# Performance work log

Measured on AMD Instinct MI355X. Metric: run time of the kernel, lower is better.

Reference implementation:

```python
import jax, jax.numpy as jnp
import numpy as np

DIM = 1024
HEADS = 16
WIN = 7
HEAD_DIM = DIM // HEADS
SCALE = HEAD_DIM ** -0.5
B = 1024
N = WIN * WIN  # 49 tokens per window


def _relative_position_index(window_size: int) -> np.ndarray:
    coords = np.stack(np.meshgrid(np.arange(window_size), np.arange(window_size), indexing='ij'))
    cf = coords.reshape(2, -1)  # [2, N]
    rel = cf[:, :, None] - cf[:, None, :]  # [2, N, N]
    rel = rel.transpose(1, 2, 0)
    rel[:, :, 0] += window_size - 1
    rel[:, :, 1] += window_size - 1
    rel[:, :, 0] *= 2 * window_size - 1
    return rel.sum(-1).astype(np.int32)  # [N, N]


def setup_inputs() -> dict:
    key = jax.random.key(0)
    ks = jax.random.split(key, 12)
    s = 0.02
    inp = {
        'landmark_features': jax.random.normal(ks[0], (B, N, DIM), jnp.float32),
        'image_features': jax.random.normal(ks[1], (B, N, DIM), jnp.float32),
        'Wq': jax.random.normal(ks[2], (DIM, DIM), jnp.float32) * s,
        'bq': jnp.zeros((DIM,), jnp.float32),
        'Wk': jax.random.normal(ks[3], (DIM, DIM), jnp.float32) * s,
        'bk': jnp.zeros((DIM,), jnp.float32),
        'Wv': jax.random.normal(ks[4], (DIM, DIM), jnp.float32) * s,
        'bv': jnp.zeros((DIM,), jnp.float32),
        'Wo': jax.random.normal(ks[5], (DIM, DIM), jnp.float32) * s,
        'bo': jnp.zeros((DIM,), jnp.float32),
        'bias_table': jax.random.normal(ks[6], ((2 * WIN - 1) ** 2, HEADS), jnp.float32) * s,
        'rel_idx': jnp.asarray(_relative_position_index(WIN)),
    }
    return inp


def reference(landmark_features, image_features, Wq, bq, Wk, bk, Wv, bv, Wo, bo, bias_table, rel_idx):
    Bsz, Nk, C = image_features.shape
    # projections (torch Linear: x @ W.T + b), split into heads -> [B, H, N, D]
    def proj(x, W, b):
        y = x @ W.T + b
        return y.reshape(Bsz, -1, HEADS, HEAD_DIM).transpose(0, 2, 1, 3)
    q = proj(landmark_features, Wq, bq)
    k = proj(image_features, Wk, bk)
    v = proj(image_features, Wv, bv)
    attn = jnp.einsum('bhqd,bhkd->bhqk', q, k) * SCALE
    # gathered relative-position bias: [H, N, N]
    bias = bias_table[rel_idx.reshape(-1)].reshape(N, N, HEADS).transpose(2, 0, 1)
    attn = attn + bias[None]
    attn = jax.nn.softmax(attn, axis=-1)
    out = jnp.einsum('bhqk,bhkd->bhqd', attn, v).transpose(0, 2, 1, 3).reshape(Bsz, -1, C)
    return out @ Wo.T + bo
```

## Files before the change

kernel.cpp:

```cpp
#include <hip/hip_runtime.h>

#define DIM 1024
#define HEADS 16
#define HEAD_DIM 64
#define NTOK 49
#define SCALEF 0.125f

typedef __attribute__((ext_vector_type(8))) short bf16x8;
typedef __attribute__((ext_vector_type(4))) float floatx4;

typedef const __attribute__((address_space(1))) void* gptr_t;
typedef __attribute__((address_space(3))) void* sptr_t;

__device__ __forceinline__ void async_load16(const void* g, void* s) {
    __builtin_amdgcn_global_load_lds((gptr_t)g, (sptr_t)s, 16, 0, 0);
}

__device__ __forceinline__ unsigned short f2bf(float f) {
    unsigned int u = __builtin_bit_cast(unsigned int, f);
    u = (u + 0x7fffu + ((u >> 16) & 1u)) >> 16;
    return (unsigned short)u;
}
__device__ __forceinline__ float bf2f(unsigned short s) {
    unsigned int u = ((unsigned int)s) << 16;
    return __builtin_bit_cast(float, u);
}

__global__ void cvt2_kernel(const float* __restrict__ a, const float* __restrict__ b,
                            unsigned short* __restrict__ oa, unsigned short* __restrict__ ob,
                            int n) {
    int i = (blockIdx.x * 256 + threadIdx.x) * 4;
    if (i >= n) return;
    float4 va = *(const float4*)&a[i];
    float4 vb = *(const float4*)&b[i];
    ushort4 ua = make_ushort4(f2bf(va.x), f2bf(va.y), f2bf(va.z), f2bf(va.w));
    ushort4 ub = make_ushort4(f2bf(vb.x), f2bf(vb.y), f2bf(vb.z), f2bf(vb.w));
    *(ushort4*)&oa[i] = ua;
    *(ushort4*)&ob[i] = ub;
}

template <bool OUT_BF16>
__global__ __launch_bounds__(256)
void gemm_bt_kernel(const unsigned short* __restrict__ A,
                    const unsigned short* __restrict__ Bw,
                    const float* __restrict__ bias,
                    void* __restrict__ Cout) {
    constexpr int K = 1024, N = 1024;
    __shared__ unsigned short As[128 * 32];
    __shared__ unsigned short Bs[128 * 32];
    const int tid = threadIdx.x;
    const int lane = tid & 63;
    const int wave = tid >> 6;
    const int wm = (wave >> 1) * 64;
    const int wn = (wave & 1) * 64;
    const int m0 = blockIdx.y * 128;
    const int n0 = blockIdx.x * 128;
    const int lr = lane & 15;
    const int lk = (lane >> 4) * 8;

    floatx4 acc[4][4] = {};

    for (int kt = 0; kt < K / 32; ++kt) {
        const int kbase = kt * 32;
#pragma unroll
        for (int j = 0; j < 2; ++j) {
            int off = tid * 16 + j * 4096;
            int r = off >> 6;
            int ce = (off & 63) >> 1;
            async_load16(A + (size_t)(m0 + r) * K + kbase + ce, (char*)As + off);
            async_load16(Bw + (size_t)(n0 + r) * K + kbase + ce, (char*)Bs + off);
        }
        __syncthreads();
        bf16x8 af[4], bfr[4];
#pragma unroll
        for (int t = 0; t < 4; ++t) {
            af[t]  = *(const bf16x8*)&As[(wm + t * 16 + lr) * 32 + lk];
            bfr[t] = *(const bf16x8*)&Bs[(wn + t * 16 + lr) * 32 + lk];
        }
#pragma unroll
        for (int mt = 0; mt < 4; ++mt)
#pragma unroll
            for (int nt = 0; nt < 4; ++nt)
                acc[mt][nt] = __builtin_amdgcn_mfma_f32_16x16x32_bf16(
                    af[mt], bfr[nt], acc[mt][nt], 0, 0, 0);
        __syncthreads();
    }

#pragma unroll
    for (int mt = 0; mt < 4; ++mt) {
#pragma unroll
        for (int nt = 0; nt < 4; ++nt) {
            int col = n0 + wn + nt * 16 + (lane & 15);
            float bv = bias[col];
#pragma unroll
            for (int r = 0; r < 4; ++r) {
                int row = m0 + wm + mt * 16 + (lane >> 4) * 4 + r;
                float v = acc[mt][nt][r] + bv;
                if (OUT_BF16)
                    ((unsigned short*)Cout)[(size_t)row * N + col] = f2bf(v);
                else
                    ((float*)Cout)[(size_t)row * N + col] = v;
            }
        }
    }
}

__global__ void bias_pre_kernel(const float* __restrict__ bias_table,
                                const int* __restrict__ rel_idx,
                                float* __restrict__ bias_dense) {
    int h = blockIdx.x;
    for (int i = threadIdx.x; i < 64 * 64; i += 256) {
        int q = i >> 6, k = i & 63;
        float v;
        if (k >= NTOK) v = -1e30f;
        else if (q >= NTOK) v = 0.f;
        else v = bias_table[rel_idx[q * NTOK + k] * HEADS + h];
        bias_dense[h * 4096 + i] = v;
    }
}

#define SWZ(row, t) ((t) ^ (((row) & 7) << 3))

__global__ __launch_bounds__(256)
void attn_mfma_kernel(const unsigned short* __restrict__ Q,
                      const unsigned short* __restrict__ K,
                      const unsigned short* __restrict__ V,
                      const float* __restrict__ bias_dense,
                      unsigned short* __restrict__ ctx) {
    __shared__ unsigned short Vt[4][64 * 64];
    __shared__ unsigned short Pm[4][64 * 64];

    const int tid = threadIdx.x;
    const int w = tid >> 6;
    const int lane = tid & 63;
    const int p = blockIdx.x * 4 + w;
    const int b = p >> 4;
    const int h = p & 15;
    const size_t base = (size_t)(b * NTOK) * DIM + h * HEAD_DIM;
    unsigned short* vt = Vt[w];
    unsigned short* pm = Pm[w];

    const int lc = lane & 15;
    const int lg = lane >> 4;

    for (int i = lane; i < 64 * 16; i += 64) {
        int tok = i >> 4, d0 = (i & 15) * 4;
        ushort4 vv = (tok < NTOK) ? *(const ushort4*)&V[base + (size_t)tok * DIM + d0]
                                  : make_ushort4(0, 0, 0, 0);
        vt[(d0 + 0) * 64 + SWZ(d0 + 0, tok)] = vv.x;
        vt[(d0 + 1) * 64 + SWZ(d0 + 1, tok)] = vv.y;
        vt[(d0 + 2) * 64 + SWZ(d0 + 2, tok)] = vv.z;
        vt[(d0 + 3) * 64 + SWZ(d0 + 3, tok)] = vv.w;
    }

    floatx4 acc[4][4] = {};
#pragma unroll
    for (int kt = 0; kt < 2; ++kt) {
        const int d = kt * 32 + lg * 8;
        bf16x8 af[4], bfr[4];
#pragma unroll
        for (int mt = 0; mt < 4; ++mt)
            af[mt] = *(const bf16x8*)&Q[base + (size_t)(mt * 16 + lc) * DIM + d];
#pragma unroll
        for (int nt = 0; nt < 4; ++nt)
            bfr[nt] = *(const bf16x8*)&K[base + (size_t)(nt * 16 + lc) * DIM + d];
#pragma unroll
        for (int mt = 0; mt < 4; ++mt)
#pragma unroll
            for (int nt = 0; nt < 4; ++nt)
                acc[mt][nt] = __builtin_amdgcn_mfma_f32_16x16x32_bf16(
                    af[mt], bfr[nt], acc[mt][nt], 0, 0, 0);
    }

    const float* bd = bias_dense + h * 4096;
#pragma unroll
    for (int mt = 0; mt < 4; ++mt) {
#pragma unroll
        for (int r = 0; r < 4; ++r) {
            const int row = mt * 16 + lg * 4 + r;
#pragma unroll
            for (int nt = 0; nt < 4; ++nt)
                acc[mt][nt][r] = acc[mt][nt][r] * SCALEF + bd[row * 64 + nt * 16 + lc];
            float mx = fmaxf(fmaxf(acc[mt][0][r], acc[mt][1][r]),
                             fmaxf(acc[mt][2][r], acc[mt][3][r]));
            mx = fmaxf(mx, __shfl_xor(mx, 1));
            mx = fmaxf(mx, __shfl_xor(mx, 2));
            mx = fmaxf(mx, __shfl_xor(mx, 4));
            mx = fmaxf(mx, __shfl_xor(mx, 8));
            float sm = 0.f;
#pragma unroll
            for (int nt = 0; nt < 4; ++nt) {
                float e = __expf(acc[mt][nt][r] - mx);
                acc[mt][nt][r] = e;
                sm += e;
            }
            sm += __shfl_xor(sm, 1);
            sm += __shfl_xor(sm, 2);
            sm += __shfl_xor(sm, 4);
            sm += __shfl_xor(sm, 8);
            const float inv = 1.f / sm;
#pragma unroll
            for (int nt = 0; nt < 4; ++nt) {
                const int col = nt * 16 + lc;
                pm[row * 64 + SWZ(row, col)] = f2bf(acc[mt][nt][r] * inv);
            }
        }
    }

    floatx4 o[4][4] = {};
#pragma unroll
    for (int kt = 0; kt < 2; ++kt) {
        const int t0 = kt * 32 + lg * 8;
        bf16x8 af[4], bfr[4];
#pragma unroll
        for (int mt = 0; mt < 4; ++mt) {
            const int q = mt * 16 + lc;
            af[mt] = *(const bf16x8*)&pm[q * 64 + SWZ(q, t0)];
        }
#pragma unroll
        for (int nt = 0; nt < 4; ++nt) {
            const int dd = nt * 16 + lc;
            bfr[nt] = *(const bf16x8*)&vt[dd * 64 + SWZ(dd, t0)];
        }
#pragma unroll
        for (int mt = 0; mt < 4; ++mt)
#pragma unroll
            for (int nt = 0; nt < 4; ++nt)
                o[mt][nt] = __builtin_amdgcn_mfma_f32_16x16x32_bf16(
                    af[mt], bfr[nt], o[mt][nt], 0, 0, 0);
    }

#pragma unroll
    for (int mt = 0; mt < 4; ++mt) {
#pragma unroll
        for (int r = 0; r < 4; ++r) {
            const int row = mt * 16 + lg * 4 + r;
            if (row < NTOK) {
#pragma unroll
                for (int nt = 0; nt < 4; ++nt)
                    ctx[base + (size_t)row * DIM + nt * 16 + lc] = f2bf(o[mt][nt][r]);
            }
        }
    }
}

extern "C" void kernel_launch(void* const* d_in, const int* in_sizes, int n_in,
                              void* d_out, int out_size, void* d_ws, size_t ws_size,
                              hipStream_t stream) {
    const float* landmark = (const float*)d_in[0];
    const float* image    = (const float*)d_in[1];
    const float* Wq = (const float*)d_in[2];
    const float* bq = (const float*)d_in[3];
    const float* Wk = (const float*)d_in[4];
    const float* bk = (const float*)d_in[5];
    const float* Wv = (const float*)d_in[6];
    const float* bv = (const float*)d_in[7];
    const float* Wo = (const float*)d_in[8];
    const float* bo = (const float*)d_in[9];
    const float* bias_table = (const float*)d_in[10];
    const int*   rel_idx    = (const int*)d_in[11];
    float* out = (float*)d_out;

    const size_t FEAT = (size_t)1024 * NTOK * DIM;
    const size_t FB   = FEAT * 2;
    const size_t WB   = (size_t)DIM * DIM * 2;
    char* ws = (char*)d_ws;
    unsigned short* Qb  = (unsigned short*)(ws + 0 * FB);
    unsigned short* Kb  = (unsigned short*)(ws + 1 * FB);
    unsigned short* Vb  = (unsigned short*)(ws + 2 * FB);
    unsigned short* Lb  = (unsigned short*)(ws + 3 * FB);
    unsigned short* Ctx = (unsigned short*)(ws + 3 * FB);
    unsigned short* Ib  = (unsigned short*)(ws + 4 * FB);
    float* bias_dense   = (float*)(ws + 4 * FB);
    unsigned short* Wqb = (unsigned short*)(ws + 5 * FB + 0 * WB);
    unsigned short* Wkb = (unsigned short*)(ws + 5 * FB + 1 * WB);
    unsigned short* Wvb = (unsigned short*)(ws + 5 * FB + 2 * WB);
    unsigned short* Wob = (unsigned short*)(ws + 5 * FB + 3 * WB);

    cvt2_kernel<<<(int)(FEAT / 4 / 256), 256, 0, stream>>>(landmark, image, Lb, Ib, (int)FEAT);
    cvt2_kernel<<<(int)(DIM * DIM / 4 / 256), 256, 0, stream>>>(Wq, Wk, Wqb, Wkb, DIM * DIM);
    cvt2_kernel<<<(int)(DIM * DIM / 4 / 256), 256, 0, stream>>>(Wv, Wo, Wvb, Wob, DIM * DIM);

    dim3 ggrid(1024 / 128, 50176 / 128);
    gemm_bt_kernel<true><<<ggrid, 256, 0, stream>>>(Lb, Wqb, bq, Qb);
    gemm_bt_kernel<true><<<ggrid, 256, 0, stream>>>(Ib, Wkb, bk, Kb);
    gemm_bt_kernel<true><<<ggrid, 256, 0, stream>>>(Ib, Wvb, bv, Vb);

    bias_pre_kernel<<<HEADS, 256, 0, stream>>>(bias_table, rel_idx, bias_dense);

    attn_mfma_kernel<<<1024 * HEADS / 4, 256, 0, stream>>>(Qb, Kb, Vb, bias_dense, Ctx);

    gemm_bt_kernel<false><<<ggrid, 256, 0, stream>>>(Ctx, Wob, bo, out);
}
```

Measured before the change: 1.324 ms.

## Rewrite attention core with 32x32 MFMA and register-resident softmax probabilities

Reworks the windowed attention kernel to compute S^T = K·Q^T with 32x32x16 bf16 MFMA, so each query's scores sit in one lane pair and softmax needs only a single cross-half shuffle. The normalized probabilities are packed into the P·V MFMA operand layout through lane shuffles, which removes the shared-memory P buffer and halves LDS use per block. The bias table is transposed to match, V loads are issued to registers before the K loads to overlap latency, and launch bounds request 4 blocks per CU. The cost is heavier register pressure from the 32-element score arrays and the fragile operand-packing logic.

```diff
diff --git a/kernel.cpp b/kernel.cpp
--- a/kernel.cpp
+++ b/kernel.cpp
@@ -8,6 +8,8 @@
 
 typedef __attribute__((ext_vector_type(8))) short bf16x8;
 typedef __attribute__((ext_vector_type(4))) float floatx4;
+typedef __attribute__((ext_vector_type(16))) float floatx16;
+typedef __attribute__((ext_vector_type(4))) unsigned int uintx4;
 
 typedef const __attribute__((address_space(1))) void* gptr_t;
 typedef __attribute__((address_space(3))) void* sptr_t;
@@ -20,10 +22,6 @@
     unsigned int u = __builtin_bit_cast(unsigned int, f);
     u = (u + 0x7fffu + ((u >> 16) & 1u)) >> 16;
     return (unsigned short)u;
-}
-__device__ __forceinline__ float bf2f(unsigned short s) {
-    unsigned int u = ((unsigned int)s) << 16;
-    return __builtin_bit_cast(float, u);
 }
 
 __global__ void cvt2_kernel(const float* __restrict__ a, const float* __restrict__ b,
@@ -107,28 +105,27 @@
 
 __global__ void bias_pre_kernel(const float* __restrict__ bias_table,
                                 const int* __restrict__ rel_idx,
-                                float* __restrict__ bias_dense) {
+                                float* __restrict__ bias_T) {
     int h = blockIdx.x;
     for (int i = threadIdx.x; i < 64 * 64; i += 256) {
-        int q = i >> 6, k = i & 63;
+        int t = i >> 6, q = i & 63;
         float v;
-        if (k >= NTOK) v = -1e30f;
+        if (t >= NTOK) v = -1e30f;
         else if (q >= NTOK) v = 0.f;
-        else v = bias_table[rel_idx[q * NTOK + k] * HEADS + h];
-        bias_dense[h * 4096 + i] = v;
+        else v = bias_table[rel_idx[q * NTOK + t] * HEADS + h];
+        bias_T[h * 4096 + i] = v;
     }
 }
 
 #define SWZ(row, t) ((t) ^ (((row) & 7) << 3))
 
-__global__ __launch_bounds__(256)
+__global__ __launch_bounds__(256, 4)
 void attn_mfma_kernel(const unsigned short* __restrict__ Q,
                       const unsigned short* __restrict__ K,
                       const unsigned short* __restrict__ V,
-                      const float* __restrict__ bias_dense,
+                      const float* __restrict__ bias_T,
                       unsigned short* __restrict__ ctx) {
     __shared__ unsigned short Vt[4][64 * 64];
-    __shared__ unsigned short Pm[4][64 * 64];
 
     const int tid = threadIdx.x;
     const int w = tid >> 6;
@@ -138,110 +135,148 @@
     const int h = p & 15;
     const size_t base = (size_t)(b * NTOK) * DIM + h * HEAD_DIM;
     unsigned short* vt = Vt[w];
-    unsigned short* pm = Pm[w];
-
-    const int lc = lane & 15;
-    const int lg = lane >> 4;
-
-    for (int i = lane; i < 64 * 16; i += 64) {
-        int tok = i >> 4, d0 = (i & 15) * 4;
-        ushort4 vv = (tok < NTOK) ? *(const ushort4*)&V[base + (size_t)tok * DIM + d0]
-                                  : make_ushort4(0, 0, 0, 0);
-        vt[(d0 + 0) * 64 + SWZ(d0 + 0, tok)] = vv.x;
-        vt[(d0 + 1) * 64 + SWZ(d0 + 1, tok)] = vv.y;
-        vt[(d0 + 2) * 64 + SWZ(d0 + 2, tok)] = vv.z;
-        vt[(d0 + 3) * 64 + SWZ(d0 + 3, tok)] = vv.w;
-    }
-
-    floatx4 acc[4][4] = {};
-#pragma unroll
-    for (int kt = 0; kt < 2; ++kt) {
-        const int d = kt * 32 + lg * 8;
-        bf16x8 af[4], bfr[4];
-#pragma unroll
-        for (int mt = 0; mt < 4; ++mt)
-            af[mt] = *(const bf16x8*)&Q[base + (size_t)(mt * 16 + lc) * DIM + d];
-#pragma unroll
-        for (int nt = 0; nt < 4; ++nt)
-            bfr[nt] = *(const bf16x8*)&K[base + (size_t)(nt * 16 + lc) * DIM + d];
-#pragma unroll
-        for (int mt = 0; mt < 4; ++mt)
-#pragma unroll
-            for (int nt = 0; nt < 4; ++nt)
-                acc[mt][nt] = __builtin_amdgcn_mfma_f32_16x16x32_bf16(
-                    af[mt], bfr[nt], acc[mt][nt], 0, 0, 0);
-    }
-
-    const float* bd = bias_dense + h * 4096;
-#pragma unroll
-    for (int mt = 0; mt < 4; ++mt) {
-#pragma unroll
-        for (int r = 0; r < 4; ++r) {
-            const int row = mt * 16 + lg * 4 + r;
-#pragma unroll
-            for (int nt = 0; nt < 4; ++nt)
-                acc[mt][nt][r] = acc[mt][nt][r] * SCALEF + bd[row * 64 + nt * 16 + lc];
-            float mx = fmaxf(fmaxf(acc[mt][0][r], acc[mt][1][r]),
-                             fmaxf(acc[mt][2][r], acc[mt][3][r]));
-            mx = fmaxf(mx, __shfl_xor(mx, 1));
-            mx = fmaxf(mx, __shfl_xor(mx, 2));
-            mx = fmaxf(mx, __shfl_xor(mx, 4));
-            mx = fmaxf(mx, __shfl_xor(mx, 8));
-            float sm = 0.f;
-#pragma unroll
-            for (int nt = 0; nt < 4; ++nt) {
-                float e = __expf(acc[mt][nt][r] - mx);
-                acc[mt][nt][r] = e;
-                sm += e;
+
+    const int l31 = lane & 31;
+    const int hi = lane >> 5;
+
+    ushort4 vreg[16];
+    const int vtok0 = lane & 15;
+    const int vd0 = (lane >> 4) * 4;
+#pragma unroll
+    for (int tb = 0; tb < 4; ++tb) {
+        const int tok = vtok0 + 16 * tb;
+        const bool valid = tok < NTOK;
+#pragma unroll
+        for (int db = 0; db < 4; ++db) {
+            const int d0 = vd0 + 16 * db;
+            vreg[tb * 4 + db] = valid ? *(const ushort4*)&V[base + (size_t)tok * DIM + d0]
+                                      : make_ushort4(0, 0, 0, 0);
+        }
+    }
+
+    bf16x8 af_k[2][4];
+#pragma unroll
+    for (int tt = 0; tt < 2; ++tt)
+#pragma unroll
+        for (int dk = 0; dk < 4; ++dk)
+            af_k[tt][dk] = *(const bf16x8*)&K[base + (size_t)(tt * 32 + l31) * DIM + dk * 16 + hi * 8];
+
+#pragma unroll
+    for (int tb = 0; tb < 4; ++tb) {
+        const int tok = vtok0 + 16 * tb;
+#pragma unroll
+        for (int db = 0; db < 4; ++db) {
+            const int d0 = vd0 + 16 * db;
+            ushort4 vv = vreg[tb * 4 + db];
+            vt[(d0 + 0) * 64 + SWZ(d0 + 0, tok)] = vv.x;
+            vt[(d0 + 1) * 64 + SWZ(d0 + 1, tok)] = vv.y;
+            vt[(d0 + 2) * 64 + SWZ(d0 + 2, tok)] = vv.z;
+            vt[(d0 + 3) * 64 + SWZ(d0 + 3, tok)] = vv.w;
+        }
+    }
+
+    const float* bT = bias_T + h * 4096;
+    uintx4 pa[2][4];
+
+#pragma unroll
+    for (int tq = 0; tq < 2; ++tq) {
+        bf16x8 bf_q[4];
+#pragma unroll
+        for (int dk = 0; dk < 4; ++dk)
+            bf_q[dk] = *(const bf16x8*)&Q[base + (size_t)(tq * 32 + l31) * DIM + dk * 16 + hi * 8];
+
+        floatx16 s[2] = {};
+#pragma unroll
+        for (int dk = 0; dk < 4; ++dk)
+#pragma unroll
+            for (int tt = 0; tt < 2; ++tt)
+                s[tt] = __builtin_amdgcn_mfma_f32_32x32x16_bf16(
+                    af_k[tt][dk], bf_q[dk], s[tt], 0, 0, 0);
+
+        float x[32];
+#pragma unroll
+        for (int tt = 0; tt < 2; ++tt)
+#pragma unroll
+            for (int r = 0; r < 16; ++r) {
+                const int t = tt * 32 + (r & 3) + 8 * (r >> 2) + 4 * hi;
+                x[tt * 16 + r] = s[tt][r] * SCALEF + bT[t * 64 + tq * 32 + l31];
             }
-            sm += __shfl_xor(sm, 1);
-            sm += __shfl_xor(sm, 2);
-            sm += __shfl_xor(sm, 4);
-            sm += __shfl_xor(sm, 8);
-            const float inv = 1.f / sm;
-#pragma unroll
-            for (int nt = 0; nt < 4; ++nt) {
-                const int col = nt * 16 + lc;
-                pm[row * 64 + SWZ(row, col)] = f2bf(acc[mt][nt][r] * inv);
+
+        float m0[16];
+#pragma unroll
+        for (int i = 0; i < 16; ++i) m0[i] = fmaxf(x[i], x[i + 16]);
+#pragma unroll
+        for (int i = 0; i < 8; ++i) m0[i] = fmaxf(m0[i], m0[i + 8]);
+#pragma unroll
+        for (int i = 0; i < 4; ++i) m0[i] = fmaxf(m0[i], m0[i + 4]);
+        float m = fmaxf(fmaxf(m0[0], m0[1]), fmaxf(m0[2], m0[3]));
+        m = fmaxf(m, __shfl_xor(m, 32));
+
+#pragma unroll
+        for (int i = 0; i < 32; ++i) x[i] = __expf(x[i] - m);
+
+        float t0s[16];
+#pragma unroll
+        for (int i = 0; i < 16; ++i) t0s[i] = x[i] + x[i + 16];
+#pragma unroll
+        for (int i = 0; i < 8; ++i) t0s[i] += t0s[i + 8];
+#pragma unroll
+        for (int i = 0; i < 4; ++i) t0s[i] += t0s[i + 4];
+        float sum = (t0s[0] + t0s[1]) + (t0s[2] + t0s[3]);
+        sum += __shfl_xor(sum, 32);
+        const float inv = 1.f / sum;
+
+#pragma unroll
+        for (int kt = 0; kt < 4; ++kt) {
+            const int B0 = (kt >> 1) * 16 + (kt & 1) * 8;
+            unsigned int a0 = ((unsigned int)f2bf(x[B0 + 1] * inv) << 16) | f2bf(x[B0 + 0] * inv);
+            unsigned int a1 = ((unsigned int)f2bf(x[B0 + 3] * inv) << 16) | f2bf(x[B0 + 2] * inv);
+            unsigned int a2 = ((unsigned int)f2bf(x[B0 + 5] * inv) << 16) | f2bf(x[B0 + 4] * inv);
+            unsigned int a3 = ((unsigned int)f2bf(x[B0 + 7] * inv) << 16) | f2bf(x[B0 + 6] * inv);
+            unsigned int s0 = __shfl_xor(a0, 32);
+            unsigned int s1 = __shfl_xor(a1, 32);
+            unsigned int s2 = __shfl_xor(a2, 32);
+            unsigned int s3 = __shfl_xor(a3, 32);
+            uintx4 wv;
+            wv[0] = hi ? s2 : a0;
+            wv[1] = hi ? s3 : a1;
+            wv[2] = hi ? a2 : s0;
+            wv[3] = hi ? a3 : s1;
+            pa[tq][kt] = wv;
+        }
+    }
+
+    floatx16 o[2][2] = {};
+#pragma unroll
+    for (int kt = 0; kt < 4; ++kt) {
+        const int t0 = kt * 16 + hi * 8;
+        bf16x8 bv[2];
+#pragma unroll
+        for (int td = 0; td < 2; ++td) {
+            const int row = td * 32 + l31;
+            bv[td] = *(const bf16x8*)&vt[row * 64 + SWZ(row, t0)];
+        }
+#pragma unroll
+        for (int tq = 0; tq < 2; ++tq) {
+            const bf16x8 ap = __builtin_bit_cast(bf16x8, pa[tq][kt]);
+#pragma unroll
+            for (int td = 0; td < 2; ++td)
+                o[tq][td] = __builtin_amdgcn_mfma_f32_32x32x16_bf16(
+                    ap, bv[td], o[tq][td], 0, 0, 0);
+        }
+    }
+
+#pragma unroll
+    for (int tq = 0; tq < 2; ++tq)
+#pragma unroll
+        for (int r = 0; r < 16; ++r) {
+            const int q = tq * 32 + (r & 3) + 8 * (r >> 2) + 4 * hi;
+            if (q < NTOK) {
+#pragma unroll
+                for (int td = 0; td < 2; ++td)
+                    ctx[base + (size_t)q * DIM + td * 32 + l31] = f2bf(o[tq][td][r]);
             }
         }
-    }
-
-    floatx4 o[4][4] = {};
-#pragma unroll
-    for (int kt = 0; kt < 2; ++kt) {
-        const int t0 = kt * 32 + lg * 8;
-        bf16x8 af[4], bfr[4];
-#pragma unroll
-        for (int mt = 0; mt < 4; ++mt) {
-            const int q = mt * 16 + lc;
-            af[mt] = *(const bf16x8*)&pm[q * 64 + SWZ(q, t0)];
-        }
-#pragma unroll
-        for (int nt = 0; nt < 4; ++nt) {
-            const int dd = nt * 16 + lc;
-            bfr[nt] = *(const bf16x8*)&vt[dd * 64 + SWZ(dd, t0)];
-        }
-#pragma unroll
-        for (int mt = 0; mt < 4; ++mt)
-#pragma unroll
-            for (int nt = 0; nt < 4; ++nt)
-                o[mt][nt] = __builtin_amdgcn_mfma_f32_16x16x32_bf16(
-                    af[mt], bfr[nt], o[mt][nt], 0, 0, 0);
-    }
-
-#pragma unroll
-    for (int mt = 0; mt < 4; ++mt) {
-#pragma unroll
-        for (int r = 0; r < 4; ++r) {
-            const int row = mt * 16 + lg * 4 + r;
-            if (row < NTOK) {
-#pragma unroll
-                for (int nt = 0; nt < 4; ++nt)
-                    ctx[base + (size_t)row * DIM + nt * 16 + lc] = f2bf(o[mt][nt][r]);
-            }
-        }
-    }
 }
 
 extern "C" void kernel_launch(void* const* d_in, const int* in_sizes, int n_in,
```

Result: faster. 1.251 ms (-5.5%).
